# Kernel optimization log

Measured on AMD Instinct MI355X. Metric: run time of the kernel, lower is better.

Reference implementation:

```python
import jax, jax.numpy as jnp
import numpy as np

DIM = 1280
HEADS = 8
DH = DIM // HEADS  # 160
CROSS = 768
FRAMES = 16
B = 2
TOK = 256        # spatial tokens per frame
ESEQ = 77
INNER = 4 * DIM  # 5120, geglu inner


def _ln(x, w, b):
    m = x.mean(-1, keepdims=True)
    v = x.var(-1, keepdims=True)
    return (x - m) / jnp.sqrt(v + 1e-5) * w + b


def _split_heads(x):
    Bt, S, C = x.shape
    return x.reshape(Bt, S, HEADS, C // HEADS).transpose(0, 2, 1, 3)


def _attn_core(q, k, v):
    # q,k,v: [B, S, C] -> multi-head attention -> [B, Sq, C]
    qh, kh, vh = _split_heads(q), _split_heads(k), _split_heads(v)
    scores = jnp.einsum('bhqd,bhkd->bhqk', qh, kh) * (DH ** -0.5)
    attn = jax.nn.softmax(scores, axis=-1)
    o = jnp.einsum('bhqk,bhkd->bhqd', attn, vh)
    Bt, H, S, Dh = o.shape
    return o.transpose(0, 2, 1, 3).reshape(Bt, S, H * Dh)


def setup_inputs() -> dict:
    key = jax.random.key(0)
    ks = jax.random.split(key, 32)
    s = 0.02

    def w(i, shape):
        return jax.random.normal(ks[i], shape, dtype=jnp.float32) * s

    inp = {
        'hidden_states': jax.random.normal(ks[0], (B * FRAMES, TOK, DIM), dtype=jnp.float32),
        'encoder_hidden_states': jax.random.normal(ks[1], (B * FRAMES, ESEQ, CROSS), dtype=jnp.float32),
        # norm1 / attn1 (sparse causal self-attn)
        'n1w': jnp.ones((DIM,), jnp.float32), 'n1b': jnp.zeros((DIM,), jnp.float32),
        'a1wq': w(2, (DIM, DIM)), 'a1wk': w(3, (DIM, DIM)), 'a1wv': w(4, (DIM, DIM)),
        'a1wo': w(5, (DIM, DIM)), 'a1bo': jnp.zeros((DIM,), jnp.float32),
        # norm2 / attn2 (cross)
        'n2w': jnp.ones((DIM,), jnp.float32), 'n2b': jnp.zeros((DIM,), jnp.float32),
        'a2wq': w(6, (DIM, DIM)), 'a2wk': w(7, (CROSS, DIM)), 'a2wv': w(8, (CROSS, DIM)),
        'a2wo': w(9, (DIM, DIM)), 'a2bo': jnp.zeros((DIM,), jnp.float32),
        # norm3 / geglu FFN
        'n3w': jnp.ones((DIM,), jnp.float32), 'n3b': jnp.zeros((DIM,), jnp.float32),
        'ffw1': w(10, (DIM, 2 * INNER)), 'ffb1': jnp.zeros((2 * INNER,), jnp.float32),
        'ffw2': w(11, (INNER, DIM)), 'ffb2': jnp.zeros((DIM,), jnp.float32),
        # norm_temp / attn_temp (temporal self-attn)
        'ntw': jnp.ones((DIM,), jnp.float32), 'ntb': jnp.zeros((DIM,), jnp.float32),
        'atwq': w(12, (DIM, DIM)), 'atwk': w(13, (DIM, DIM)), 'atwv': w(14, (DIM, DIM)),
        'atwo': w(15, (DIM, DIM)), 'atbo': jnp.zeros((DIM,), jnp.float32),
        'video_length': FRAMES,
    }
    return inp


def reference(hidden_states, encoder_hidden_states,
              n1w, n1b, a1wq, a1wk, a1wv, a1wo, a1bo,
              n2w, n2b, a2wq, a2wk, a2wv, a2wo, a2bo,
              n3w, n3b, ffw1, ffb1, ffw2, ffb2,
              ntw, ntb, atwq, atwk, atwv, atwo, atbo,
              video_length):
    f = video_length
    bf, d, c = hidden_states.shape
    b = bf // f
    h = hidden_states

    # ---- attn1: sparse causal self-attention ----
    nh = _ln(h, n1w, n1b)
    q = nh @ a1wq                                   # [bf, d, c]
    k = (nh @ a1wk).reshape(b, f, d, c)
    v = (nh @ a1wv).reshape(b, f, d, c)
    former = jnp.maximum(jnp.arange(f) - 1, 0)      # clamp(arange-1, min=0)
    k_sel = jnp.concatenate([jnp.broadcast_to(k[:, :1], (b, f, d, c)), k[:, former]], axis=2)
    v_sel = jnp.concatenate([jnp.broadcast_to(v[:, :1], (b, f, d, c)), v[:, former]], axis=2)
    k_sel = k_sel.reshape(bf, 2 * d, c)
    v_sel = v_sel.reshape(bf, 2 * d, c)
    h = _attn_core(q, k_sel, v_sel) @ a1wo + a1bo + h

    # ---- attn2: cross-attention to text ----
    nh = _ln(h, n2w, n2b)
    h = _attn_core(nh @ a2wq, encoder_hidden_states @ a2wk, encoder_hidden_states @ a2wv) @ a2wo + a2bo + h

    # ---- geglu FFN ----
    nh = _ln(h, n3w, n3b)
    pg = nh @ ffw1 + ffb1
    p, g = jnp.split(pg, 2, axis=-1)
    h = (p * jax.nn.gelu(g, approximate=False)) @ ffw2 + ffb2 + h

    # ---- temporal self-attention over frames ----
    ht = h.reshape(b, f, d, c).transpose(0, 2, 1, 3).reshape(b * d, f, c)
    nh = _ln(ht, ntw, ntb)
    ht = _attn_core(nh @ atwq, nh @ atwk, nh @ atwv) @ atwo + atbo + ht
    h = ht.reshape(b, d, f, c).transpose(0, 2, 1, 3).reshape(bf, d, c)
    return h
```

## Files before the change

kernel.cpp:

```cpp
#include <hip/hip_runtime.h>
#include <hip/hip_bf16.h>
#include <math.h>

#define DIM    1280
#define HEADS  8
#define DH     160
#define FRAMES 16
#define BATCH  2
#define TOK    256
#define ESEQ   77
#define INNER  5120
#define CROSS  768
#define BF     (BATCH*FRAMES)
#define ROWS   (BF*TOK)
#define EROWS  (BF*ESEQ)
#define EPAD   2560

typedef __hip_bfloat16 bf16;
typedef __attribute__((ext_vector_type(8))) short s8v;
typedef __attribute__((ext_vector_type(4))) short s4v;
typedef __attribute__((ext_vector_type(4))) float f4v;

__device__ __forceinline__ float us2f(unsigned short u) {
    union { float f; unsigned int i; } c; c.i = ((unsigned int)u) << 16; return c.f;
}
__device__ __forceinline__ float b2f(bf16 x) { return __bfloat162float(x); }
__device__ __forceinline__ bf16  f2b(float x) { return __float2bfloat16(x); }
__device__ __forceinline__ short f2s(float x) {
    union { float f; unsigned int u; } c; c.f = x;
    unsigned int r = c.u + 0x7FFF + ((c.u >> 16) & 1);
    return (short)(r >> 16);
}
__device__ __forceinline__ void load4(const float* p, float* d) {
    float4 v = *(const float4*)p; d[0] = v.x; d[1] = v.y; d[2] = v.z; d[3] = v.w;
}
__device__ __forceinline__ void gl_lds16(const bf16* g, short* l) {
    __builtin_amdgcn_global_load_lds(
        (const __attribute__((address_space(1))) void*)g,
        (__attribute__((address_space(3))) void*)l, 16, 0, 0);
}

__global__ __launch_bounds__(256) void ln_kernel(const float* __restrict__ x,
                                                 const float* __restrict__ w,
                                                 const float* __restrict__ b,
                                                 bf16* __restrict__ out) {
    __shared__ float r1[256], r2[256];
    int row = blockIdx.x, t = threadIdx.x;
    const float* xp = x + (size_t)row * DIM;
    float v[5], s = 0.f, s2 = 0.f;
#pragma unroll
    for (int i = 0; i < 5; i++) {
        float xv = xp[t + 256 * i];
        v[i] = xv; s += xv; s2 += xv * xv;
    }
    r1[t] = s; r2[t] = s2; __syncthreads();
    for (int st = 128; st > 0; st >>= 1) {
        if (t < st) { r1[t] += r1[t + st]; r2[t] += r2[t + st]; }
        __syncthreads();
    }
    float mean = r1[0] * (1.f / DIM);
    float var  = r2[0] * (1.f / DIM) - mean * mean;
    float rstd = rsqrtf(var + 1e-5f);
    bf16* op = out + (size_t)row * DIM;
#pragma unroll
    for (int i = 0; i < 5; i++) {
        int c = t + 256 * i;
        op[c] = f2b((v[i] - mean) * rstd * w[c] + b[c]);
    }
}

__global__ __launch_bounds__(256) void wconv_t(const float* __restrict__ w,
                                               bf16* __restrict__ wt,
                                               int N, int K) {
    __shared__ float tile[64][65];
    const int n0 = blockIdx.x * 64, k0 = blockIdx.y * 64;
    const int t = threadIdx.x;
    const int tr = t >> 4;
    const int tc = (t & 15) * 4;
#pragma unroll
    for (int i = 0; i < 4; i++) {
        int kk = tr + i * 16;
        float4 vv = *(const float4*)(w + (size_t)(k0 + kk) * N + n0 + tc);
        tile[kk][tc + 0] = vv.x; tile[kk][tc + 1] = vv.y;
        tile[kk][tc + 2] = vv.z; tile[kk][tc + 3] = vv.w;
    }
    __syncthreads();
#pragma unroll
    for (int i = 0; i < 4; i++) {
        int nn = tr + i * 16;
        s4v o4 = (s4v){ f2s(tile[tc + 0][nn]), f2s(tile[tc + 1][nn]),
                        f2s(tile[tc + 2][nn]), f2s(tile[tc + 3][nn]) };
        *(s4v*)(wt + (size_t)(n0 + nn) * K + k0 + tc) = o4;
    }
}

__global__ __launch_bounds__(256) void wconv_t4(const float* __restrict__ w0,
                                                const float* __restrict__ w1,
                                                const float* __restrict__ w2,
                                                const float* __restrict__ w3,
                                                bf16* __restrict__ wt, size_t dstride,
                                                int N, int K) {
    const float* w = blockIdx.z == 0 ? w0 : blockIdx.z == 1 ? w1
                   : blockIdx.z == 2 ? w2 : w3;
    bf16* dst = wt + (size_t)blockIdx.z * dstride;
    __shared__ float tile[64][65];
    const int n0 = blockIdx.x * 64, k0 = blockIdx.y * 64;
    const int t = threadIdx.x;
    const int tr = t >> 4;
    const int tc = (t & 15) * 4;
#pragma unroll
    for (int i = 0; i < 4; i++) {
        int kk = tr + i * 16;
        float4 vv = *(const float4*)(w + (size_t)(k0 + kk) * N + n0 + tc);
        tile[kk][tc + 0] = vv.x; tile[kk][tc + 1] = vv.y;
        tile[kk][tc + 2] = vv.z; tile[kk][tc + 3] = vv.w;
    }
    __syncthreads();
#pragma unroll
    for (int i = 0; i < 4; i++) {
        int nn = tr + i * 16;
        s4v o4 = (s4v){ f2s(tile[tc + 0][nn]), f2s(tile[tc + 1][nn]),
                        f2s(tile[tc + 2][nn]), f2s(tile[tc + 3][nn]) };
        *(s4v*)(dst + (size_t)(n0 + nn) * K + k0 + tc) = o4;
    }
}

__global__ __launch_bounds__(256) void encconv(const float* __restrict__ e,
                                               bf16* __restrict__ eb) {
    int idx = blockIdx.x * 256 + threadIdx.x;
    int base = idx * 4;
    int row = base / CROSS;
    s4v o4;
    if (row < EROWS) {
        float4 vv = *(const float4*)(e + (size_t)base);
        o4 = (s4v){ f2s(vv.x), f2s(vv.y), f2s(vv.z), f2s(vv.w) };
    } else {
        o4 = (s4v){ 0, 0, 0, 0 };
    }
    *(s4v*)(eb + base) = o4;
}

template <int EPI>
__global__ __launch_bounds__(512, 2) void gemm_bt8(
    const bf16* __restrict__ A, int lda,
    const bf16* __restrict__ Bt, int ldb,
    void* __restrict__ C, int ldc,
    const float* __restrict__ bias,
    const float* __restrict__ res, int ldres,
    int M, int N, int K) {
    __shared__ short lds[2][2][256 * 64];

    const int t = threadIdx.x;
    const int wid = t >> 6, lane = t & 63;
    const int lrow = lane & 15, lgrp = lane >> 4;
    const int wr = wid >> 2, wc = wid & 3;
    const int m0 = blockIdx.y * 256, n0 = blockIdx.x * 256;

    f4v acc[8][4];
#pragma unroll
    for (int i = 0; i < 8; i++)
#pragma unroll
        for (int j = 0; j < 4; j++) acc[i][j] = (f4v){0.f, 0.f, 0.f, 0.f};

    const int srow = wid * 32 + (lane >> 3);
    const int scol = (((lane & 7) - (lane >> 3)) & 7) * 8;
    const bf16* Ag = A + (size_t)(m0 + srow) * lda + scol;
    const bf16* Bg = Bt + (size_t)(n0 + srow) * ldb + scol;

    auto stage = [&](int b, int kt) {
#pragma unroll
        for (int s = 0; s < 4; s++) {
            gl_lds16(Ag + (size_t)kt * 64 + (size_t)(s * 8) * lda,
                     &lds[b][0][wid * 2048 + s * 512]);
            gl_lds16(Bg + (size_t)kt * 64 + (size_t)(s * 8) * ldb,
                     &lds[b][1][wid * 2048 + s * 512]);
        }
    };

    const int KT = K >> 6;
    stage(0, 0);
    __syncthreads();
    int buf = 0;
    for (int kt = 0; kt < KT; kt++, buf ^= 1) {
        if (kt + 1 < KT) stage(buf ^ 1, kt + 1);
#pragma unroll
        for (int ks = 0; ks < 2; ks++) {
            const int cc = ((ks * 4 + lgrp + lrow) & 7) * 8;
            s8v bfr[4];
#pragma unroll
            for (int j = 0; j < 4; j++)
                bfr[j] = *(const s8v*)&lds[buf][1][(wc * 64 + j * 16 + lrow) * 64 + cc];
#pragma unroll
            for (int i = 0; i < 8; i++) {
                s8v af = *(const s8v*)&lds[buf][0][(wr * 128 + i * 16 + lrow) * 64 + cc];
#pragma unroll
                for (int j = 0; j < 4; j++)
                    acc[i][j] = __builtin_amdgcn_mfma_f32_16x16x32_bf16(af, bfr[j], acc[i][j], 0, 0, 0);
            }
        }
        __syncthreads();
    }

    float bs[4];
    if (EPI == 1) {
#pragma unroll
        for (int j = 0; j < 4; j++) bs[j] = bias[n0 + wc * 64 + j * 16 + lrow];
    }
#pragma unroll
    for (int i = 0; i < 8; i++) {
#pragma unroll
        for (int r = 0; r < 4; r++) {
            int m = m0 + wr * 128 + i * 16 + lgrp * 4 + r;
#pragma unroll
            for (int j = 0; j < 4; j++) {
                int n = n0 + wc * 64 + j * 16 + lrow;
                float v = acc[i][j][r];
                if (EPI == 0) {
                    ((bf16*)C)[(size_t)m * ldc + n] = f2b(v);
                } else {
                    ((float*)C)[(size_t)m * ldc + n] = v + bs[j] + res[(size_t)m * ldres + n];
                }
            }
        }
    }
}

template <int EPI>
__global__ __launch_bounds__(256) void gemm_bt(
    const bf16* __restrict__ A, int lda,
    const bf16* __restrict__ Bt, int ldb,
    void* __restrict__ C, int ldc,
    const float* __restrict__ bias,
    const float* __restrict__ res, int ldres,
    int M, int N, int K) {
    constexpr int BN = (EPI == 2) ? 64 : 128;
    constexpr int MI = (EPI == 2) ? 2 : 4;
    __shared__ short A_lds[2][128 * 32];
    __shared__ short B_lds[2][BN * 32];
    __shared__ short G_lds[EPI == 2 ? 2 * 64 * 32 : 8];

    const int t = threadIdx.x;
    const int wid = t >> 6, lane = t & 63;
    const int lrow = lane & 15, lgrp = lane >> 4;
    const int m0 = blockIdx.y * 128, n0 = blockIdx.x * BN;
    const int wm = (EPI == 2) ? wid * 32 : (wid & 1) * 64;
    const int wn = (EPI == 2) ? 0 : (wid >> 1) * 64;

    f4v acc[MI][4];
    f4v accg[EPI == 2 ? MI : 1][4];
#pragma unroll
    for (int i = 0; i < MI; i++)
#pragma unroll
        for (int j = 0; j < 4; j++) {
            acc[i][j] = (f4v){0.f, 0.f, 0.f, 0.f};
            if (EPI == 2) accg[i][j] = (f4v){0.f, 0.f, 0.f, 0.f};
        }

    const int scol = (lane & 3) * 8;
    const int arow = wid * 32 + (lane >> 2);
    const int brow = (EPI == 2) ? (wid * 16 + (lane >> 2)) : arow;
    const bf16* Ag0 = A + (size_t)(m0 + arow) * lda + scol;
    const bf16* Bg0 = Bt + (size_t)(n0 + brow) * ldb + scol;
    const bf16* Gg0 = (EPI == 2) ? (Bt + (size_t)(INNER + n0 + brow) * ldb + scol) : Bg0;

    auto stage = [&](int buf, int kk) {
        gl_lds16(Ag0 + kk, &A_lds[buf][wid * 1024]);
        gl_lds16(Ag0 + kk + (size_t)16 * lda, &A_lds[buf][wid * 1024 + 512]);
        if constexpr (EPI == 2) {
            gl_lds16(Bg0 + kk, &B_lds[buf][wid * 512]);
            gl_lds16(Gg0 + kk, &G_lds[buf * 2048 + wid * 512]);
        } else {
            gl_lds16(Bg0 + kk, &B_lds[buf][wid * 1024]);
            gl_lds16(Bg0 + kk + (size_t)16 * ldb, &B_lds[buf][wid * 1024 + 512]);
        }
    };

    stage(0, 0);
    __syncthreads();
    int buf = 0;
    for (int k0 = 0; k0 < K; k0 += 32, buf ^= 1) {
        if (k0 + 32 < K) stage(buf ^ 1, k0 + 32);

        s8v af[MI], bfr[4];
#pragma unroll
        for (int i = 0; i < MI; i++)
            af[i] = *(const s8v*)&A_lds[buf][(wm + i * 16 + lrow) * 32 + lgrp * 8];
#pragma unroll
        for (int j = 0; j < 4; j++)
            bfr[j] = *(const s8v*)&B_lds[buf][(wn + j * 16 + lrow) * 32 + lgrp * 8];
#pragma unroll
        for (int i = 0; i < MI; i++)
#pragma unroll
            for (int j = 0; j < 4; j++)
                acc[i][j] = __builtin_amdgcn_mfma_f32_16x16x32_bf16(af[i], bfr[j], acc[i][j], 0, 0, 0);
        if constexpr (EPI == 2) {
            s8v gfr[4];
#pragma unroll
            for (int j = 0; j < 4; j++)
                gfr[j] = *(const s8v*)&G_lds[buf * 2048 + (j * 16 + lrow) * 32 + lgrp * 8];
#pragma unroll
            for (int i = 0; i < MI; i++)
#pragma unroll
                for (int j = 0; j < 4; j++)
                    accg[i][j] = __builtin_amdgcn_mfma_f32_16x16x32_bf16(af[i], gfr[j], accg[i][j], 0, 0, 0);
        }
        __syncthreads();
    }

#pragma unroll
    for (int i = 0; i < MI; i++) {
#pragma unroll
        for (int r = 0; r < 4; r++) {
            int m = m0 + wm + i * 16 + lgrp * 4 + r;
#pragma unroll
            for (int j = 0; j < 4; j++) {
                int n = n0 + wn + j * 16 + lrow;
                float v = acc[i][j][r];
                if (EPI == 0) {
                    ((bf16*)C)[(size_t)m * ldc + n] = f2b(v);
                } else if (EPI == 1) {
                    v += bias[n] + res[(size_t)m * ldres + n];
                    ((float*)C)[(size_t)m * ldc + n] = v;
                } else {
                    float p = v + bias[n];
                    float g = accg[i][j][r] + bias[INNER + n];
                    float gl = 0.5f * g * (1.f + erff(g * 0.70710678118654752f));
                    ((bf16*)C)[(size_t)m * ldc + n] = f2b(p * gl);
                }
            }
        }
    }
}

template <int EPI>
__global__ __launch_bounds__(256) void gemm_mfma(
    const bf16* __restrict__ A, int lda,
    const float* __restrict__ B, int ldb,
    void* __restrict__ C, int ldc,
    const float* __restrict__ bias,
    const float* __restrict__ res, int ldres,
    int M, int N, int K) {
    constexpr int LR = 40;
    __shared__ short A_lds[128 * LR];
    __shared__ short B_lds[128 * LR];
    __shared__ short G_lds[EPI == 2 ? 128 * LR : 4];

    const int t    = threadIdx.x;
    const int wid  = t >> 6, lane = t & 63;
    const int lrow = lane & 15, lgrp = lane >> 4;
    const int m0   = blockIdx.y * 128, n0 = blockIdx.x * 128;
    const int wm   = (wid & 1) * 64, wn = (wid >> 1) * 64;

    f4v acc[4][4];
    f4v accg[4][4];
#pragma unroll
    for (int i = 0; i < 4; i++)
#pragma unroll
        for (int j = 0; j < 4; j++) {
            acc[i][j] = (f4v){0.f, 0.f, 0.f, 0.f};
            if (EPI == 2) accg[i][j] = (f4v){0.f, 0.f, 0.f, 0.f};
        }

    const int b_np = (t & 31) * 4;
    const int b_kp = (t >> 5) * 4;

    for (int k0 = 0; k0 < K; k0 += 32) {
#pragma unroll
        for (int c = 0; c < 2; c++) {
            int idx = t + c * 256;
            int row = idx >> 2, g = (idx & 3) * 8;
            uint4 v = *(const uint4*)(A + (size_t)(m0 + row) * lda + k0 + g);
            *(uint4*)&A_lds[row * LR + g] = v;
        }
        {
            const float* bp = B + (size_t)(k0 + b_kp) * ldb + n0 + b_np;
            float4 r0 = *(const float4*)(bp);
            float4 r1 = *(const float4*)(bp + ldb);
            float4 r2 = *(const float4*)(bp + 2 * ldb);
            float4 r3 = *(const float4*)(bp + 3 * ldb);
            *(s4v*)&B_lds[(b_np + 0) * LR + b_kp] = (s4v){f2s(r0.x), f2s(r1.x), f2s(r2.x), f2s(r3.x)};
            *(s4v*)&B_lds[(b_np + 1) * LR + b_kp] = (s4v){f2s(r0.y), f2s(r1.y), f2s(r2.y), f2s(r3.y)};
            *(s4v*)&B_lds[(b_np + 2) * LR + b_kp] = (s4v){f2s(r0.z), f2s(r1.z), f2s(r2.z), f2s(r3.z)};
            *(s4v*)&B_lds[(b_np + 3) * LR + b_kp] = (s4v){f2s(r0.w), f2s(r1.w), f2s(r2.w), f2s(r3.w)};
        }
        if (EPI == 2) {
            const float* gp = B + (size_t)(k0 + b_kp) * ldb + INNER + n0 + b_np;
            float4 r0 = *(const float4*)(gp);
            float4 r1 = *(const float4*)(gp + ldb);
            float4 r2 = *(const float4*)(gp + 2 * ldb);
            float4 r3 = *(const float4*)(gp + 3 * ldb);
            *(s4v*)&G_lds[(b_np + 0) * LR + b_kp] = (s4v){f2s(r0.x), f2s(r1.x), f2s(r2.x), f2s(r3.x)};
            *(s4v*)&G_lds[(b_np + 1) * LR + b_kp] = (s4v){f2s(r0.y), f2s(r1.y), f2s(r2.y), f2s(r3.y)};
            *(s4v*)&G_lds[(b_np + 2) * LR + b_kp] = (s4v){f2s(r0.z), f2s(r1.z), f2s(r2.z), f2s(r3.z)};
            *(s4v*)&G_lds[(b_np + 3) * LR + b_kp] = (s4v){f2s(r0.w), f2s(r1.w), f2s(r2.w), f2s(r3.w)};
        }
        __syncthreads();
        s8v af[4], bfr[4];
#pragma unroll
        for (int i = 0; i < 4; i++)
            af[i] = *(const s8v*)&A_lds[(wm + i * 16 + lrow) * LR + lgrp * 8];
#pragma unroll
        for (int j = 0; j < 4; j++)
            bfr[j] = *(const s8v*)&B_lds[(wn + j * 16 + lrow) * LR + lgrp * 8];
#pragma unroll
        for (int i = 0; i < 4; i++)
#pragma unroll
            for (int j = 0; j < 4; j++)
                acc[i][j] = __builtin_amdgcn_mfma_f32_16x16x32_bf16(af[i], bfr[j], acc[i][j], 0, 0, 0);
        if (EPI == 2) {
            s8v gfr[4];
#pragma unroll
            for (int j = 0; j < 4; j++)
                gfr[j] = *(const s8v*)&G_lds[(wn + j * 16 + lrow) * LR + lgrp * 8];
#pragma unroll
            for (int i = 0; i < 4; i++)
#pragma unroll
                for (int j = 0; j < 4; j++)
                    accg[i][j] = __builtin_amdgcn_mfma_f32_16x16x32_bf16(af[i], gfr[j], accg[i][j], 0, 0, 0);
        }
        __syncthreads();
    }
#pragma unroll
    for (int i = 0; i < 4; i++) {
#pragma unroll
        for (int r = 0; r < 4; r++) {
            int m = m0 + wm + i * 16 + lgrp * 4 + r;
#pragma unroll
            for (int j = 0; j < 4; j++) {
                int n = n0 + wn + j * 16 + lrow;
                float v = acc[i][j][r];
                if (EPI == 0) {
                    ((bf16*)C)[(size_t)m * ldc + n] = f2b(v);
                } else if (EPI == 1) {
                    v += bias[n] + res[(size_t)m * ldres + n];
                    ((float*)C)[(size_t)m * ldc + n] = v;
                } else {
                    float p = v + bias[n];
                    float g = accg[i][j][r] + bias[INNER + n];
                    float gl = 0.5f * g * (1.f + erff(g * 0.70710678118654752f));
                    ((bf16*)C)[(size_t)m * ldc + n] = f2b(p * gl);
                }
            }
        }
    }
}

__global__ __launch_bounds__(256) void gemm_valu(
    const float* __restrict__ A, int lda,
    const float* __restrict__ B, int ldb,
    bf16* __restrict__ C, int ldc,
    int M, int N, int K) {
    __shared__ float As[16][65];
    __shared__ float Bs[16][65];
    const int t  = threadIdx.x;
    const int m0 = blockIdx.y * 64, n0 = blockIdx.x * 64;
    const int ar = t >> 2, ak = (t & 3) * 4;
    const int bk = t >> 4, bn = (t & 15) * 4;
    const int ty = t >> 4, tx = t & 15;
    float acc[4][4];
#pragma unroll
    for (int i = 0; i < 4; i++)
#pragma unroll
        for (int j = 0; j < 4; j++) acc[i][j] = 0.f;

    for (int k0 = 0; k0 < K; k0 += 16) {
        {
            int m = m0 + ar;
            float tmp[4];
            if (m < M) load4(A + (size_t)m * lda + k0 + ak, tmp);
            else { tmp[0] = tmp[1] = tmp[2] = tmp[3] = 0.f; }
            As[ak + 0][ar] = tmp[0]; As[ak + 1][ar] = tmp[1];
            As[ak + 2][ar] = tmp[2]; As[ak + 3][ar] = tmp[3];
        }
        {
            float tmp[4];
            load4(B + (size_t)(k0 + bk) * ldb + n0 + bn, tmp);
            Bs[bk][bn + 0] = tmp[0]; Bs[bk][bn + 1] = tmp[1];
            Bs[bk][bn + 2] = tmp[2]; Bs[bk][bn + 3] = tmp[3];
        }
        __syncthreads();
#pragma unroll
        for (int k = 0; k < 16; k++) {
            float a[4], b[4];
#pragma unroll
            for (int i = 0; i < 4; i++) a[i] = As[k][ty * 4 + i];
#pragma unroll
            for (int j = 0; j < 4; j++) b[j] = Bs[k][tx * 4 + j];
#pragma unroll
            for (int i = 0; i < 4; i++)
#pragma unroll
                for (int j = 0; j < 4; j++) acc[i][j] += a[i] * b[j];
        }
        __syncthreads();
    }
#pragma unroll
    for (int i = 0; i < 4; i++) {
        int m = m0 + ty * 4 + i;
        if (m >= M) continue;
#pragma unroll
        for (int j = 0; j < 4; j++) {
            int n = n0 + tx * 4 + j;
            C[(size_t)m * ldc + n] = f2b(acc[i][j]);
        }
    }
}

#define SOFTMAX_SCALE 0.07905694150420949f

#define A1_KP 168
#define A1_VP 72
#define A1_PP 72

__global__ __launch_bounds__(256) void attn1_mfma(const bf16* __restrict__ q,
                                                  const bf16* __restrict__ k,
                                                  const bf16* __restrict__ v,
                                                  int ldq,
                                                  bf16* __restrict__ o) {
    __shared__ short K_lds[64 * A1_KP];
    __shared__ short Vt_lds[160 * A1_VP];
    __shared__ short P_lds[4 * 16 * A1_PP];

    const int t = threadIdx.x;
    const int wid = t >> 6, lane = t & 63;
    const int lrow = lane & 15, lgrp = lane >> 4;
    const int bx = blockIdx.x, hd = blockIdx.y, bfi = blockIdx.z;
    const int bi = bfi >> 4, fi = bfi & 15;
    const int former = fi > 0 ? fi - 1 : 0;
    const int qrow0 = bfi * TOK + bx * 64 + wid * 16;

    s8v qf[5];
    {
        const bf16* qp = q + (size_t)(qrow0 + lrow) * ldq + hd * DH + lgrp * 8;
#pragma unroll
        for (int ks = 0; ks < 5; ks++)
            qf[ks] = *(const s8v*)(qp + ks * 32);
    }

    f4v oacc[10];
#pragma unroll
    for (int dg = 0; dg < 10; dg++) oacc[dg] = (f4v){0.f, 0.f, 0.f, 0.f};
    float m_run[4], l_run[4];
#pragma unroll
    for (int r = 0; r < 4; r++) { m_run[r] = -1e30f; l_run[r] = 0.f; }

    short* P_w = P_lds + wid * 16 * A1_PP;

    for (int c = 0; c < 8; c++) {
        const int kf = (c < 4) ? 0 : former;
        const size_t krow0 = (size_t)(bi * FRAMES + kf) * TOK + (c & 3) * 64;

        __syncthreads();
#pragma unroll
        for (int it = 0; it < 5; it++) {
            int idx = t + it * 256;
            int jr = idx / 20, g = idx % 20;
            const bf16* kp = k + (krow0 + jr) * ldq + hd * DH + g * 8;
            *(uint4*)&K_lds[jr * A1_KP + g * 8] = *(const uint4*)kp;
            s8v vv = *(const s8v*)(v + (krow0 + jr) * ldq + hd * DH + g * 8);
#pragma unroll
            for (int i = 0; i < 8; i++) {
                int d = g * 8 + i;
                Vt_lds[d * A1_VP + (jr ^ (d & 56))] = vv[i];
            }
        }
        __syncthreads();

        f4v sacc[4];
#pragma unroll
        for (int kg = 0; kg < 4; kg++) {
            sacc[kg] = (f4v){0.f, 0.f, 0.f, 0.f};
#pragma unroll
            for (int ks = 0; ks < 5; ks++) {
                s8v kfr = *(const s8v*)&K_lds[(kg * 16 + lrow) * A1_KP + ks * 32 + lgrp * 8];
                sacc[kg] = __builtin_amdgcn_mfma_f32_16x16x32_bf16(qf[ks], kfr, sacc[kg], 0, 0, 0);
            }
        }

        float mc[4];
#pragma unroll
        for (int r = 0; r < 4; r++) {
            float mm = fmaxf(fmaxf(sacc[0][r], sacc[1][r]), fmaxf(sacc[2][r], sacc[3][r]));
            mc[r] = mm * SOFTMAX_SCALE;
        }
#pragma unroll
        for (int x = 1; x < 16; x <<= 1)
#pragma unroll
            for (int r = 0; r < 4; r++)
                mc[r] = fmaxf(mc[r], __shfl_xor(mc[r], x));

        float p[4][4], rs[4];
#pragma unroll
        for (int r = 0; r < 4; r++) {
            float mn = fmaxf(m_run[r], mc[r]);
            float sc = __expf(m_run[r] - mn);
            m_run[r] = mn;
            l_run[r] *= sc;
#pragma unroll
            for (int dg = 0; dg < 10; dg++) oacc[dg][r] *= sc;
            float acc = 0.f;
#pragma unroll
            for (int kg = 0; kg < 4; kg++) {
                float e = __expf(sacc[kg][r] * SOFTMAX_SCALE - mn);
                p[kg][r] = e; acc += e;
            }
            rs[r] = acc;
        }
#pragma unroll
        for (int x = 1; x < 16; x <<= 1)
#pragma unroll
            for (int r = 0; r < 4; r++)
                rs[r] += __shfl_xor(rs[r], x);
#pragma unroll
        for (int r = 0; r < 4; r++) l_run[r] += rs[r];

#pragma unroll
        for (int kg = 0; kg < 4; kg++)
#pragma unroll
            for (int r = 0; r < 4; r++)
                P_w[(lgrp * 4 + r) * A1_PP + kg * 16 + lrow] = f2s(p[kg][r]);
        __syncthreads();

        s8v pa[2];
#pragma unroll
        for (int ks2 = 0; ks2 < 2; ks2++)
            pa[ks2] = *(const s8v*)&P_w[lrow * A1_PP + ks2 * 32 + lgrp * 8];
#pragma unroll
        for (int dg = 0; dg < 10; dg++) {
            int dd = dg * 16 + lrow;
#pragma unroll
            for (int ks2 = 0; ks2 < 2; ks2++) {
                s8v vfr = *(const s8v*)&Vt_lds[dd * A1_VP + ((ks2 * 32 + lgrp * 8) ^ (dd & 56))];
                oacc[dg] = __builtin_amdgcn_mfma_f32_16x16x32_bf16(pa[ks2], vfr, oacc[dg], 0, 0, 0);
            }
        }
    }

    float invl[4];
#pragma unroll
    for (int r = 0; r < 4; r++) invl[r] = 1.f / l_run[r];
#pragma unroll
    for (int dg = 0; dg < 10; dg++) {
#pragma unroll
        for (int r = 0; r < 4; r++) {
            int qq = qrow0 + lgrp * 4 + r;
            o[(size_t)qq * DIM + hd * DH + dg * 16 + lrow] = f2b(oacc[dg][r] * invl[r]);
        }
    }
}

__global__ __launch_bounds__(256) void attn2_mfma(const bf16* __restrict__ q,
                                                  const bf16* __restrict__ k,
                                                  const bf16* __restrict__ v,
                                                  int ldk,
                                                  bf16* __restrict__ o) {
    __shared__ short K_lds[64 * A1_KP];
    __shared__ short Vt_lds[160 * A1_VP];
    __shared__ short P_lds[4 * 16 * A1_PP];

    const int t = threadIdx.x;
    const int wid = t >> 6, lane = t & 63;
    const int lrow = lane & 15, lgrp = lane >> 4;
    const int bx = blockIdx.x, hd = blockIdx.y, bfi = blockIdx.z;
    const int qrow0 = bfi * TOK + bx * 64 + wid * 16;

    s8v qf[5];
    {
        const bf16* qp = q + (size_t)(qrow0 + lrow) * DIM + hd * DH + lgrp * 8;
#pragma unroll
        for (int ks = 0; ks < 5; ks++)
            qf[ks] = *(const s8v*)(qp + ks * 32);
    }

    f4v oacc[10];
#pragma unroll
    for (int dg = 0; dg < 10; dg++) oacc[dg] = (f4v){0.f, 0.f, 0.f, 0.f};
    float m_run[4], l_run[4];
#pragma unroll
    for (int r = 0; r < 4; r++) { m_run[r] = -1e30f; l_run[r] = 0.f; }

    short* P_w = P_lds + wid * 16 * A1_PP;

    for (int c = 0; c < 2; c++) {
        const size_t krow0 = (size_t)bfi * ESEQ + c * 64;

        __syncthreads();
#pragma unroll
        for (int it = 0; it < 5; it++) {
            int idx = t + it * 256;
            int jr = idx / 20, g = idx % 20;
            const bf16* kp = k + (krow0 + jr) * ldk + hd * DH + g * 8;
            *(uint4*)&K_lds[jr * A1_KP + g * 8] = *(const uint4*)kp;
            s8v vv = *(const s8v*)(v + (krow0 + jr) * ldk + hd * DH + g * 8);
#pragma unroll
            for (int i = 0; i < 8; i++) {
                int d = g * 8 + i;
                Vt_lds[d * A1_VP + (jr ^ (d & 56))] = vv[i];
            }
        }
        __syncthreads();

        f4v sacc[4];
#pragma unroll
        for (int kg = 0; kg < 4; kg++) {
            sacc[kg] = (f4v){0.f, 0.f, 0.f, 0.f};
#pragma unroll
            for (int ks = 0; ks < 5; ks++) {
                s8v kfr = *(const s8v*)&K_lds[(kg * 16 + lrow) * A1_KP + ks * 32 + lgrp * 8];
                sacc[kg] = __builtin_amdgcn_mfma_f32_16x16x32_bf16(qf[ks], kfr, sacc[kg], 0, 0, 0);
            }
            if (c == 1 && (kg > 0 || lrow >= 13))
                sacc[kg] = (f4v){-1e30f, -1e30f, -1e30f, -1e30f};
        }

        float mc[4];
#pragma unroll
        for (int r = 0; r < 4; r++) {
            float mm = fmaxf(fmaxf(sacc[0][r], sacc[1][r]), fmaxf(sacc[2][r], sacc[3][r]));
            mc[r] = mm * SOFTMAX_SCALE;
        }
#pragma unroll
        for (int x = 1; x < 16; x <<= 1)
#pragma unroll
            for (int r = 0; r < 4; r++)
                mc[r] = fmaxf(mc[r], __shfl_xor(mc[r], x));

        float p[4][4], rs[4];
#pragma unroll
        for (int r = 0; r < 4; r++) {
            float mn = fmaxf(m_run[r], mc[r]);
            float sc = __expf(m_run[r] - mn);
            m_run[r] = mn;
            l_run[r] *= sc;
#pragma unroll
            for (int dg = 0; dg < 10; dg++) oacc[dg][r] *= sc;
            float acc = 0.f;
#pragma unroll
            for (int kg = 0; kg < 4; kg++) {
                float e = __expf(sacc[kg][r] * SOFTMAX_SCALE - mn);
                p[kg][r] = e; acc += e;
            }
            rs[r] = acc;
        }
#pragma unroll
        for (int x = 1; x < 16; x <<= 1)
#pragma unroll
            for (int r = 0; r < 4; r++)
                rs[r] += __shfl_xor(rs[r], x);
#pragma unroll
        for (int r = 0; r < 4; r++) l_run[r] += rs[r];

#pragma unroll
        for (int kg = 0; kg < 4; kg++)
#pragma unroll
            for (int r = 0; r < 4; r++)
                P_w[(lgrp * 4 + r) * A1_PP + kg * 16 + lrow] = f2s(p[kg][r]);
        __syncthreads();

        s8v pa[2];
#pragma unroll
        for (int ks2 = 0; ks2 < 2; ks2++)
            pa[ks2] = *(const s8v*)&P_w[lrow * A1_PP + ks2 * 32 + lgrp * 8];
#pragma unroll
        for (int dg = 0; dg < 10; dg++) {
            int dd = dg * 16 + lrow;
#pragma unroll
            for (int ks2 = 0; ks2 < 2; ks2++) {
                s8v vfr = *(const s8v*)&Vt_lds[dd * A1_VP + ((ks2 * 32 + lgrp * 8) ^ (dd & 56))];
                oacc[dg] = __builtin_amdgcn_mfma_f32_16x16x32_bf16(pa[ks2], vfr, oacc[dg], 0, 0, 0);
            }
        }
    }

    float invl[4];
#pragma unroll
    for (int r = 0; r < 4; r++) invl[r] = 1.f / l_run[r];
#pragma unroll
    for (int dg = 0; dg < 10; dg++) {
#pragma unroll
        for (int r = 0; r < 4; r++) {
            int qq = qrow0 + lgrp * 4 + r;
            o[(size_t)qq * DIM + hd * DH + dg * 16 + lrow] = f2b(oacc[dg][r] * invl[r]);
        }
    }
}

__global__ __launch_bounds__(256) void attn2_kernel(const bf16* __restrict__ q,
                                                    const bf16* __restrict__ k,
                                                    const bf16* __restrict__ v,
                                                    bf16* __restrict__ o) {
    __shared__ float sQ[DH];
    __shared__ float sS[128];
    __shared__ float red[256];
    int t = threadIdx.x;
    int qi = blockIdx.x, hd = blockIdx.y, bfi = blockIdx.z;
    size_t qbase = ((size_t)(bfi * TOK + qi)) * DIM + hd * DH;
    if (t < DH) sQ[t] = b2f(q[qbase + t]);
    __syncthreads();
    if (t < ESEQ) {
        size_t kbase = ((size_t)(bfi * ESEQ + t)) * DIM + hd * DH;
        float acc = 0.f;
        for (int d = 0; d < DH; d++) acc += sQ[d] * b2f(k[kbase + d]);
        sS[t] = acc * SOFTMAX_SCALE;
    }
    __syncthreads();
    float lm = (t < ESEQ) ? sS[t] : -1e30f;
    red[t] = lm; __syncthreads();
    for (int s = 128; s > 0; s >>= 1) { if (t < s) red[t] = fmaxf(red[t], red[t + s]); __syncthreads(); }
    float mx = red[0]; __syncthreads();
    float ls = 0.f;
    if (t < ESEQ) { float e = __expf(sS[t] - mx); sS[t] = e; ls = e; }
    red[t] = ls; __syncthreads();
    for (int s = 128; s > 0; s >>= 1) { if (t < s) red[t] += red[t + s]; __syncthreads(); }
    float inv = 1.f / red[0];
    __syncthreads();
    if (t < DH) {
        float acc = 0.f;
        for (int j = 0; j < ESEQ; j++) {
            size_t vbase = ((size_t)(bfi * ESEQ + j)) * DIM + hd * DH;
            acc += sS[j] * b2f(v[vbase + t]);
        }
        o[qbase + t] = f2b(acc * inv);
    }
}

#define AT_P 168
__global__ __launch_bounds__(256) void attnt_vec(const bf16* __restrict__ q,
                                                 const bf16* __restrict__ k,
                                                 const bf16* __restrict__ v,
                                                 int ldq,
                                                 bf16* __restrict__ o) {
    __shared__ short Q_l[16 * AT_P], K_l[16 * AT_P], V_l[16 * AT_P];
    __shared__ float P_l[16][17];
    const int t = threadIdx.x;
    const int hd = blockIdx.y;
    const int z = blockIdx.x;
    const int bi = z >> 8, ti = z & 255;

#pragma unroll
    for (int it = 0; it < 2; it++) {
        int c = t + it * 256;
        if (c < 320) {
            int f = c / 20, g = c % 20;
            size_t row = (size_t)(bi * FRAMES + f) * TOK + ti;
            const bf16* qp = q + row * ldq + hd * DH + g * 8;
            const bf16* kp = k + row * ldq + hd * DH + g * 8;
            const bf16* vp = v + row * ldq + hd * DH + g * 8;
            *(uint4*)&Q_l[f * AT_P + g * 8] = *(const uint4*)qp;
            *(uint4*)&K_l[f * AT_P + g * 8] = *(const uint4*)kp;
            *(uint4*)&V_l[f * AT_P + g * 8] = *(const uint4*)vp;
        }
    }
    __syncthreads();

    const int fq = t >> 4, fk = t & 15;
    float acc = 0.f;
#pragma unroll
    for (int dg = 0; dg < 20; dg++) {
        s8v qv = *(const s8v*)&Q_l[fq * AT_P + dg * 8];
        s8v kv = *(const s8v*)&K_l[fk * AT_P + dg * 8];
#pragma unroll
        for (int e = 0; e < 8; e++)
            acc += us2f((unsigned short)qv[e]) * us2f((unsigned short)kv[e]);
    }
    acc *= SOFTMAX_SCALE;
    float mx = acc;
#pragma unroll
    for (int x = 1; x < 16; x <<= 1) mx = fmaxf(mx, __shfl_xor(mx, x));
    float ex = __expf(acc - mx);
    float sm = ex;
#pragma unroll
    for (int x = 1; x < 16; x <<= 1) sm += __shfl_xor(sm, x);
    P_l[fq][fk] = ex / sm;
    __syncthreads();

#pragma unroll
    for (int it = 0; it < 2; it++) {
        int a = t + it * 256;
        if (a < 320) {
            int pq = a & 15, dg = a >> 4;
            float pr[16];
#pragma unroll
            for (int j = 0; j < 16; j++) pr[j] = P_l[pq][j];
            float ov[8] = {0.f, 0.f, 0.f, 0.f, 0.f, 0.f, 0.f, 0.f};
#pragma unroll
            for (int j = 0; j < 16; j++) {
                s8v vv = *(const s8v*)&V_l[j * AT_P + dg * 8];
#pragma unroll
                for (int i = 0; i < 8; i++)
                    ov[i] += pr[j] * us2f((unsigned short)vv[i]);
            }
            s8v o8;
#pragma unroll
            for (int i = 0; i < 8; i++) o8[i] = f2s(ov[i]);
            size_t orow = (size_t)(bi * FRAMES + pq) * TOK + ti;
            *(s8v*)(o + orow * DIM + hd * DH + dg * 8) = o8;
        }
    }
}

__global__ __launch_bounds__(256) void attnt_kernel(const bf16* __restrict__ q,
                                                    const bf16* __restrict__ k,
                                                    const bf16* __restrict__ v,
                                                    int ldq,
                                                    bf16* __restrict__ o) {
    __shared__ float sQ[DH];
    __shared__ float sS[16];
    __shared__ float red[256];
    int t = threadIdx.x;
    int qfi = blockIdx.x, hd = blockIdx.y, z = blockIdx.z;
    int bi = z >> 8, ti = z & 255;
    size_t qrow = (size_t)(bi * FRAMES + qfi) * TOK + ti;
    if (t < DH) sQ[t] = b2f(q[qrow * ldq + hd * DH + t]);
    __syncthreads();
    if (t < FRAMES) {
        size_t krow = (size_t)(bi * FRAMES + t) * TOK + ti;
        float acc = 0.f;
        for (int d = 0; d < DH; d++) acc += sQ[d] * b2f(k[krow * ldq + hd * DH + d]);
        sS[t] = acc * SOFTMAX_SCALE;
    }
    __syncthreads();
    float lm = (t < FRAMES) ? sS[t] : -1e30f;
    red[t] = lm; __syncthreads();
    for (int s = 128; s > 0; s >>= 1) { if (t < s) red[t] = fmaxf(red[t], red[t + s]); __syncthreads(); }
    float mx = red[0]; __syncthreads();
    float ls = 0.f;
    if (t < FRAMES) { float e = __expf(sS[t] - mx); sS[t] = e; ls = e; }
    red[t] = ls; __syncthreads();
    for (int s = 128; s > 0; s >>= 1) { if (t < s) red[t] += red[t + s]; __syncthreads(); }
    float inv = 1.f / red[0];
    __syncthreads();
    if (t < DH) {
        float acc = 0.f;
        for (int j = 0; j < FRAMES; j++) {
            size_t vrow = (size_t)(bi * FRAMES + j) * TOK + ti;
            acc += sS[j] * b2f(v[vrow * ldq + hd * DH + t]);
        }
        o[qrow * DIM + hd * DH + t] = f2b(acc * inv);
    }
}

extern "C" void kernel_launch(void* const* d_in, const int* in_sizes, int n_in,
                              void* d_out, int out_size, void* d_ws, size_t ws_size,
                              hipStream_t stream) {
    (void)in_sizes; (void)n_in; (void)out_size;
    const float* hs   = (const float*)d_in[0];
    const float* enc  = (const float*)d_in[1];
    const float* n1w  = (const float*)d_in[2];
    const float* n1b  = (const float*)d_in[3];
    const float* a1wq = (const float*)d_in[4];
    const float* a1wk = (const float*)d_in[5];
    const float* a1wv = (const float*)d_in[6];
    const float* a1wo = (const float*)d_in[7];
    const float* a1bo = (const float*)d_in[8];
    const float* n2w  = (const float*)d_in[9];
    const float* n2b  = (const float*)d_in[10];
    const float* a2wq = (const float*)d_in[11];
    const float* a2wk = (const float*)d_in[12];
    const float* a2wv = (const float*)d_in[13];
    const float* a2wo = (const float*)d_in[14];
    const float* a2bo = (const float*)d_in[15];
    const float* n3w  = (const float*)d_in[16];
    const float* n3b  = (const float*)d_in[17];
    const float* ffw1 = (const float*)d_in[18];
    const float* ffb1 = (const float*)d_in[19];
    const float* ffw2 = (const float*)d_in[20];
    const float* ffb2 = (const float*)d_in[21];
    const float* ntw  = (const float*)d_in[22];
    const float* ntb  = (const float*)d_in[23];
    const float* atwq = (const float*)d_in[24];
    const float* atwk = (const float*)d_in[25];
    const float* atwv = (const float*)d_in[26];
    const float* atwo = (const float*)d_in[27];
    const float* atbo = (const float*)d_in[28];

    char* wp = (char*)d_ws;
    auto carve = [&](size_t bytes) -> char* {
        char* p = wp; wp += (bytes + 255) & ~((size_t)255); return p;
    };
    const size_t BUF = (size_t)ROWS * DIM * 2;
    const size_t W_FULL = 26214400;
    float* out = (float*)d_out;
    dim3 blk(256);
    dim3 blk8(512);

    bf16* nh = (bf16*)carve(BUF);

    bool full = (ws_size >= 5 * BUF + W_FULL + 4096);
    if (!full) {
        bf16* qb = (bf16*)carve(BUF);
        bf16* kb = (bf16*)carve(BUF);
        bf16* vb = (bf16*)carve(BUF);
        bf16* ob = (bf16*)carve(BUF);
        bf16* Pb = qb;
        auto proj = [&](const bf16* A, int lda, const float* B, int ldb,
                        bf16* C, int ldc, int M, int N, int K) {
            gemm_mfma<0><<<dim3(N / 128, M / 128), blk, 0, stream>>>(
                A, lda, B, ldb, C, ldc, nullptr, nullptr, 0, M, N, K);
        };
        auto outproj = [&](const bf16* A, int lda, const float* B,
                           const float* bias, const float* res, int K) {
            gemm_mfma<1><<<dim3(DIM / 128, ROWS / 128), blk, 0, stream>>>(
                A, lda, B, DIM, out, DIM, bias, res, DIM, ROWS, DIM, K);
        };
        ln_kernel<<<dim3(ROWS), blk, 0, stream>>>(hs, n1w, n1b, nh);
        proj(nh, DIM, a1wq, DIM, qb, DIM, ROWS, DIM, DIM);
        proj(nh, DIM, a1wk, DIM, kb, DIM, ROWS, DIM, DIM);
        proj(nh, DIM, a1wv, DIM, vb, DIM, ROWS, DIM, DIM);
        attn1_mfma<<<dim3(TOK / 64, HEADS, BF), blk, 0, stream>>>(qb, kb, vb, DIM, ob);
        outproj(ob, DIM, a1wo, a1bo, hs, DIM);

        ln_kernel<<<dim3(ROWS), blk, 0, stream>>>(out, n2w, n2b, nh);
        proj(nh, DIM, a2wq, DIM, qb, DIM, ROWS, DIM, DIM);
        gemm_valu<<<dim3(DIM / 64, (EROWS + 63) / 64), blk, 0, stream>>>(enc, CROSS, a2wk, DIM, kb, DIM, EROWS, DIM, CROSS);
        gemm_valu<<<dim3(DIM / 64, (EROWS + 63) / 64), blk, 0, stream>>>(enc, CROSS, a2wv, DIM, vb, DIM, EROWS, DIM, CROSS);
        attn2_kernel<<<dim3(TOK, HEADS, BF), blk, 0, stream>>>(qb, kb, vb, ob);
        outproj(ob, DIM, a2wo, a2bo, out, DIM);

        ln_kernel<<<dim3(ROWS), blk, 0, stream>>>(out, n3w, n3b, nh);
        gemm_mfma<2><<<dim3(INNER / 128, ROWS / 128), blk, 0, stream>>>(
            nh, DIM, ffw1, 2 * INNER, Pb, INNER, ffb1, nullptr, 0, ROWS, INNER, DIM);
        outproj(Pb, INNER, ffw2, ffb2, out, INNER);

        ln_kernel<<<dim3(ROWS), blk, 0, stream>>>(out, ntw, ntb, nh);
        proj(nh, DIM, atwq, DIM, qb, DIM, ROWS, DIM, DIM);
        proj(nh, DIM, atwk, DIM, kb, DIM, ROWS, DIM, DIM);
        proj(nh, DIM, atwv, DIM, vb, DIM, ROWS, DIM, DIM);
        attnt_kernel<<<dim3(FRAMES, HEADS, BATCH * TOK), blk, 0, stream>>>(qb, kb, vb, DIM, ob);
        outproj(ob, DIM, atwo, atbo, out, DIM);
        return;
    }

    bf16* C3 = (bf16*)carve(3 * BUF);
    bf16* ob = (bf16*)carve(BUF);
    bf16* Ws = (bf16*)carve(W_FULL);
    bf16* Pb = C3;
    const size_t WQ = (size_t)DIM * DIM;
    const size_t WC = (size_t)DIM * CROSS;
    const int LDQ3 = 3 * DIM;

    auto projN = [&](const bf16* A, int lda, const bf16* Bt, int ldb,
                     bf16* C, int ldc, int M, int N, int K) {
        gemm_bt8<0><<<dim3(N / 256, M / 256), blk8, 0, stream>>>(
            A, lda, Bt, ldb, C, ldc, nullptr, nullptr, 0, M, N, K);
    };
    auto outprojN = [&](const bf16* A, int lda, const bf16* Bt, int ldb,
                        const float* bias, const float* res, int K) {
        gemm_bt8<1><<<dim3(DIM / 256, ROWS / 256), blk8, 0, stream>>>(
            A, lda, Bt, ldb, out, DIM, bias, res, DIM, ROWS, DIM, K);
    };

    wconv_t4<<<dim3(DIM / 64, DIM / 64, 4), blk, 0, stream>>>(
        a1wq, a1wk, a1wv, a1wo, Ws, WQ, DIM, DIM);
    ln_kernel<<<dim3(ROWS), blk, 0, stream>>>(hs, n1w, n1b, nh);
    projN(nh, DIM, Ws, DIM, C3, LDQ3, ROWS, 3 * DIM, DIM);
    attn1_mfma<<<dim3(TOK / 64, HEADS, BF), blk, 0, stream>>>(
        C3, C3 + DIM, C3 + 2 * DIM, LDQ3, ob);
    outprojN(ob, DIM, Ws + 3 * WQ, DIM, a1bo, hs, DIM);

    {
        bf16* w2q  = Ws;
        bf16* w2o  = Ws + WQ;
        bf16* w2k  = Ws + 2 * WQ;
        bf16* w2v  = w2k + WC;
        bf16* encb = w2v + WC;
        bf16* qb2  = C3;
        bf16* kv2  = C3 + (size_t)ROWS * DIM;
        wconv_t4<<<dim3(DIM / 64, DIM / 64, 2), blk, 0, stream>>>(
            a2wq, a2wo, nullptr, nullptr, w2q, WQ, DIM, DIM);
        wconv_t4<<<dim3(DIM / 64, CROSS / 64, 2), blk, 0, stream>>>(
            a2wk, a2wv, nullptr, nullptr, w2k, WC, DIM, CROSS);
        encconv<<<dim3(EPAD * CROSS / 1024), blk, 0, stream>>>(enc, encb);
        ln_kernel<<<dim3(ROWS), blk, 0, stream>>>(out, n2w, n2b, nh);
        projN(nh, DIM, w2q, DIM, qb2, DIM, ROWS, DIM, DIM);
        projN(encb, CROSS, w2k, CROSS, kv2, 2 * DIM, EPAD, 2 * DIM, CROSS);
        attn2_mfma<<<dim3(TOK / 64, HEADS, BF), blk, 0, stream>>>(
            qb2, kv2, kv2 + DIM, 2 * DIM, ob);
        outprojN(ob, DIM, w2o, DIM, a2bo, out, DIM);
    }

    wconv_t<<<dim3(2 * INNER / 64, DIM / 64), blk, 0, stream>>>(ffw1, Ws, 2 * INNER, DIM);
    ln_kernel<<<dim3(ROWS), blk, 0, stream>>>(out, n3w, n3b, nh);
    gemm_bt<2><<<dim3(INNER / 64, ROWS / 128), blk, 0, stream>>>(
        nh, DIM, Ws, DIM, Pb, INNER, ffb1, nullptr, 0, ROWS, INNER, DIM);
    wconv_t<<<dim3(DIM / 64, INNER / 64), blk, 0, stream>>>(ffw2, Ws, DIM, INNER);
    gemm_bt8<1><<<dim3(DIM / 256, ROWS / 256), blk8, 0, stream>>>(
        Pb, INNER, Ws, INNER, out, DIM, ffb2, out, DIM, ROWS, DIM, INNER);

    wconv_t4<<<dim3(DIM / 64, DIM / 64, 4), blk, 0, stream>>>(
        atwq, atwk, atwv, atwo, Ws, WQ, DIM, DIM);
    ln_kernel<<<dim3(ROWS), blk, 0, stream>>>(out, ntw, ntb, nh);
    projN(nh, DIM, Ws, DIM, C3, LDQ3, ROWS, 3 * DIM, DIM);
    attnt_vec<<<dim3(BATCH * TOK, HEADS), blk, 0, stream>>>(
        C3, C3 + DIM, C3 + 2 * DIM, LDQ3, ob);
    outprojN(ob, DIM, Ws + 3 * WQ, DIM, atbo, out, DIM);
}
```

Before: 1.191 ms.

## Add 512-thread large-tile GEGLU GEMM kernel with fused gelu epilogue

Replaces the 256-thread GEGLU projection GEMM (128x64 tile) with a new 512-thread kernel that computes a 256x128 output tile of both the value and gate halves, using 64-wide K stages with swizzled LDS and double buffering. The larger tile raises arithmetic intensity and reuse of the A operand across both halves. It applies bias and exact erf-gelu gating in the epilogue. The cost is high register pressure from 32 accumulator vectors per thread and large LDS use, which may limit occupancy despite the launch bound of 2 blocks.

```diff
diff --git a/kernel.cpp b/kernel.cpp
--- a/kernel.cpp
+++ b/kernel.cpp
@@ -220,6 +220,104 @@
                 } else {
                     ((float*)C)[(size_t)m * ldc + n] = v + bs[j] + res[(size_t)m * ldres + n];
                 }
+            }
+        }
+    }
+}
+
+__global__ __launch_bounds__(512, 2) void gemm_bt8g(
+    const bf16* __restrict__ A, int lda,
+    const bf16* __restrict__ Bt, int ldb,
+    bf16* __restrict__ C, int ldc,
+    const float* __restrict__ bias,
+    int M, int N, int K) {
+    __shared__ short A_lds[2][256 * 64];
+    __shared__ short P_ldsb[2][128 * 64];
+    __shared__ short G_ldsb[2][128 * 64];
+
+    const int t = threadIdx.x;
+    const int wid = t >> 6, lane = t & 63;
+    const int lrow = lane & 15, lgrp = lane >> 4;
+    const int wr = wid >> 2, wc = wid & 3;
+    const int m0 = blockIdx.y * 256, n0 = blockIdx.x * 128;
+
+    f4v accp[8][2], accg[8][2];
+#pragma unroll
+    for (int i = 0; i < 8; i++)
+#pragma unroll
+        for (int j = 0; j < 2; j++) {
+            accp[i][j] = (f4v){0.f, 0.f, 0.f, 0.f};
+            accg[i][j] = (f4v){0.f, 0.f, 0.f, 0.f};
+        }
+
+    const int scol = (((lane & 7) - (lane >> 3)) & 7) * 8;
+    const int arow = wid * 32 + (lane >> 3);
+    const int brow = wid * 16 + (lane >> 3);
+    const bf16* Ag = A + (size_t)(m0 + arow) * lda + scol;
+    const bf16* Pg = Bt + (size_t)(n0 + brow) * ldb + scol;
+    const bf16* Gg = Bt + (size_t)(INNER + n0 + brow) * ldb + scol;
+
+    auto stage = [&](int b, int kt) {
+#pragma unroll
+        for (int s = 0; s < 4; s++)
+            gl_lds16(Ag + (size_t)kt * 64 + (size_t)(s * 8) * lda,
+                     &A_lds[b][wid * 2048 + s * 512]);
+#pragma unroll
+        for (int s = 0; s < 2; s++) {
+            gl_lds16(Pg + (size_t)kt * 64 + (size_t)(s * 8) * ldb,
+                     &P_ldsb[b][wid * 1024 + s * 512]);
+            gl_lds16(Gg + (size_t)kt * 64 + (size_t)(s * 8) * ldb,
+                     &G_ldsb[b][wid * 1024 + s * 512]);
+        }
+    };
+
+    const int KT = K >> 6;
+    stage(0, 0);
+    __syncthreads();
+    int buf = 0;
+    for (int kt = 0; kt < KT; kt++, buf ^= 1) {
+        if (kt + 1 < KT) stage(buf ^ 1, kt + 1);
+#pragma unroll
+        for (int ks = 0; ks < 2; ks++) {
+            const int cc = ((ks * 4 + lgrp + lrow) & 7) * 8;
+            s8v pf[2], gf[2];
+#pragma unroll
+            for (int j = 0; j < 2; j++) {
+                pf[j] = *(const s8v*)&P_ldsb[buf][(wc * 32 + j * 16 + lrow) * 64 + cc];
+                gf[j] = *(const s8v*)&G_ldsb[buf][(wc * 32 + j * 16 + lrow) * 64 + cc];
+            }
+#pragma unroll
+            for (int i = 0; i < 8; i++) {
+                s8v af = *(const s8v*)&A_lds[buf][(wr * 128 + i * 16 + lrow) * 64 + cc];
+#pragma unroll
+                for (int j = 0; j < 2; j++) {
+                    accp[i][j] = __builtin_amdgcn_mfma_f32_16x16x32_bf16(af, pf[j], accp[i][j], 0, 0, 0);
+                    accg[i][j] = __builtin_amdgcn_mfma_f32_16x16x32_bf16(af, gf[j], accg[i][j], 0, 0, 0);
+                }
+            }
+        }
+        __syncthreads();
+    }
+
+    float bp[2], bg[2];
+#pragma unroll
+    for (int j = 0; j < 2; j++) {
+        int n = n0 + wc * 32 + j * 16 + lrow;
+        bp[j] = bias[n];
+        bg[j] = bias[INNER + n];
+    }
+#pragma unroll
+    for (int i = 0; i < 8; i++) {
+#pragma unroll
+        for (int r = 0; r < 4; r++) {
+            int m = m0 + wr * 128 + i * 16 + lgrp * 4 + r;
+#pragma unroll
+            for (int j = 0; j < 2; j++) {
+                int n = n0 + wc * 32 + j * 16 + lrow;
+                float p = accp[i][j][r] + bp[j];
+                float g = accg[i][j][r] + bg[j];
+                float gl = 0.5f * g * (1.f + erff(g * 0.70710678118654752f));
+                C[(size_t)m * ldc + n] = f2b(p * gl);
             }
         }
     }
@@ -1080,8 +1178,8 @@
 
     wconv_t<<<dim3(2 * INNER / 64, DIM / 64), blk, 0, stream>>>(ffw1, Ws, 2 * INNER, DIM);
     ln_kernel<<<dim3(ROWS), blk, 0, stream>>>(out, n3w, n3b, nh);
-    gemm_bt<2><<<dim3(INNER / 64, ROWS / 128), blk, 0, stream>>>(
-        nh, DIM, Ws, DIM, Pb, INNER, ffb1, nullptr, 0, ROWS, INNER, DIM);
+    gemm_bt8g<<<dim3(INNER / 128, ROWS / 256), blk8, 0, stream>>>(
+        nh, DIM, Ws, DIM, Pb, INNER, ffb1, ROWS, INNER, DIM);
     wconv_t<<<dim3(DIM / 64, INNER / 64), blk, 0, stream>>>(ffw2, Ws, DIM, INNER);
     gemm_bt8<1><<<dim3(DIM / 256, ROWS / 256), blk8, 0, stream>>>(
         Pb, INNER, Ws, INNER, out, DIM, ffb2, out, DIM, ROWS, DIM, INNER);
```

New measurement: 1.145 ms. 3.8% less time.
